# Kernel tuning notes

Measured on AMD Instinct MI355X. Metric: run time of the kernel, lower is better.

## Reference

```python
import jax, jax.numpy as jnp
import numpy as np

N_NODES = 100000
N_EDGES = 1600000
IN_CH = 48
OUT_CH = 48
BN_EPS = 1e-5


def setup_inputs() -> dict:
    key = jax.random.key(0)
    k1, k2, k3, k4 = jax.random.split(key, 4)
    x = jax.random.normal(k1, (N_NODES, IN_CH), dtype=jnp.float32)
    edge_index = jax.random.randint(k2, (2, N_EDGES), 0, N_NODES, dtype=jnp.int32)
    # GCNConv linear weight (glorot) and bias
    W = jax.random.normal(k3, (IN_CH, OUT_CH), dtype=jnp.float32) * (1.0 / np.sqrt(IN_CH))
    b = jnp.zeros((OUT_CH,), dtype=jnp.float32)
    # BatchNorm affine params
    gamma = jnp.ones((OUT_CH,), dtype=jnp.float32)
    beta = jnp.zeros((OUT_CH,), dtype=jnp.float32)
    return {"x": x, "edge_index": edge_index, "W": W, "b": b, "gamma": gamma, "beta": beta}


def reference(x, edge_index, W, b, gamma, beta):
    N = x.shape[0]
    # --- GCNConv: add self loops ---
    loops = jnp.arange(N, dtype=edge_index.dtype)
    src = jnp.concatenate([edge_index[0], loops])
    dst = jnp.concatenate([edge_index[1], loops])
    # symmetric normalization: deg counted at destination (incl. self loops)
    deg = jax.ops.segment_sum(jnp.ones_like(dst, dtype=x.dtype), dst, num_segments=N)
    dinv = jax.lax.rsqrt(deg)  # deg >= 1 due to self loops
    norm = dinv[src] * dinv[dst]  # [E+N]
    # linear transform first (small GEMM), then gather-scale-scatter
    h = x @ W  # [N, OUT_CH]
    msg = h[src] * norm[:, None]  # [E+N, OUT_CH]
    agg = jax.ops.segment_sum(msg, dst, num_segments=N) + b  # [N, OUT_CH]
    # --- BatchNorm1d (training mode: batch statistics, biased variance) ---
    mean = jnp.mean(agg, axis=0)
    var = jnp.mean(jnp.square(agg - mean), axis=0)
    y = (agg - mean) * jax.lax.rsqrt(var + BN_EPS) * gamma + beta
    # --- ReLU ---
    return jax.nn.relu(y)
```

## Files before the change

kernel.cpp:

```cpp
#include <hip/hip_runtime.h>
#include <hip/hip_bf16.h>

#define IN_CH 48
#define OUT_CH 48
#define BN_EPS 1e-5f
#define CHUNK 4096
#define EPT   16
#define NPB   256
#define NHB   512

__device__ __forceinline__ float bf2f(ushort u) {
    union { unsigned int i; float f; } v;
    v.i = ((unsigned int)u) << 16;
    return v.f;
}
__device__ __forceinline__ ushort f2bf(float f) {
    __hip_bfloat16 h = __float2bfloat16(f);
    return *(ushort*)&h;
}

__global__ __launch_bounds__(512) void k_zero(int* __restrict__ bhist) {
    bhist[threadIdx.x] = 0;
}

__global__ __launch_bounds__(256) void k_binhist(const int* __restrict__ dst,
                                                 int* __restrict__ bhist, int E) {
    __shared__ int h[512];
    int t = threadIdx.x;
    h[t] = 0; h[t + 256] = 0;
    __syncthreads();
    const int stride = NHB * 256;
    int e = blockIdx.x * 256 + t;
    for (; e + 3 * stride < E; e += 4 * stride) {
        int d0 = dst[e];
        int d1 = dst[e + stride];
        int d2 = dst[e + 2 * stride];
        int d3 = dst[e + 3 * stride];
        atomicAdd(&h[d0 >> 8], 1);
        atomicAdd(&h[d1 >> 8], 1);
        atomicAdd(&h[d2 >> 8], 1);
        atomicAdd(&h[d3 >> 8], 1);
    }
    for (; e < E; e += stride) atomicAdd(&h[dst[e] >> 8], 1);
    __syncthreads();
    if (h[t]) atomicAdd(&bhist[t], h[t]);
    if (h[t + 256]) atomicAdd(&bhist[t + 256], h[t + 256]);
}

__global__ __launch_bounds__(256) void k_scanb(const int* __restrict__ bhist,
                                               int* __restrict__ bstart,
                                               int* __restrict__ bcur, int nb,
                                               float* __restrict__ stats) {
    __shared__ int sc[256];
    int t = threadIdx.x;
    if (t < 128) stats[t] = 0.0f;
    int i0 = 2 * t, i1 = 2 * t + 1;
    int a0 = bhist[i0];
    int a1 = bhist[i1];
    int ps = a0 + a1;
    sc[t] = ps;
    __syncthreads();
    for (int off = 1; off < 256; off <<= 1) {
        int v = (t >= off) ? sc[t - off] : 0;
        __syncthreads();
        sc[t] += v;
        __syncthreads();
    }
    int excl = sc[t] - ps;
    bstart[i0] = excl;
    bstart[i1] = excl + a0;
    if (i0 < nb) bcur[i0] = excl;
    if (i1 < nb) bcur[i1] = excl + a0;
    if (t == 255) bstart[512] = sc[255];
}

union alignas(16) SMem {
    struct {
        int hist[512];
        int hbase[513];
        int sc[256];
        int gb[512];
        unsigned int stage[CHUNK];
        short stagebk[CHUNK];
    } bin;
    float Wl[IN_CH * OUT_CH];
};

__global__ __launch_bounds__(256) void k_binmm(const int* __restrict__ src,
                                               const int* __restrict__ dst,
                                               int* __restrict__ bcur,
                                               unsigned int* __restrict__ binned,
                                               int E, int nchunks,
                                               const float* __restrict__ x,
                                               const float* __restrict__ W,
                                               ushort* __restrict__ g, int N) {
    __shared__ SMem sm;
    int t = threadIdx.x;

    if (blockIdx.x < nchunks) {
        int e0 = blockIdx.x * CHUNK;
        int n = min(CHUNK, E - e0);

        sm.bin.hist[t] = 0; sm.bin.hist[t + 256] = 0;
        __syncthreads();

        unsigned int w[EPT];
        short bb[EPT];
#pragma unroll
        for (int k = 0; k < EPT; ++k) {
            int i = t + k * 256;
            if (i < n) {
                int e = e0 + i;
                int s = src[e], d = dst[e];
                int b = d >> 8;
                w[k] = (unsigned int)s | ((unsigned int)(d & 255) << 17);
                bb[k] = (short)b;
                atomicAdd(&sm.bin.hist[b], 1);
            } else bb[k] = -1;
        }
        __syncthreads();
        int a0 = sm.bin.hist[2 * t], a1 = sm.bin.hist[2 * t + 1];
        int ps = a0 + a1;
        sm.bin.sc[t] = ps;
        __syncthreads();
        for (int off = 1; off < 256; off <<= 1) {
            int v = (t >= off) ? sm.bin.sc[t - off] : 0;
            __syncthreads();
            sm.bin.sc[t] += v;
            __syncthreads();
        }
        int excl = sm.bin.sc[t] - ps;
        sm.bin.hbase[2 * t] = excl;
        sm.bin.hbase[2 * t + 1] = excl + a0;
        if (t == 255) sm.bin.hbase[512] = sm.bin.sc[255];
        __syncthreads();
        sm.bin.hist[2 * t] = excl;
        sm.bin.hist[2 * t + 1] = excl + a0;
        __syncthreads();
#pragma unroll
        for (int k = 0; k < EPT; ++k) {
            if (bb[k] >= 0) {
                int pos = atomicAdd(&sm.bin.hist[bb[k]], 1);
                sm.bin.stage[pos] = w[k];
                sm.bin.stagebk[pos] = bb[k];
            }
        }
        __syncthreads();
        for (int b = t; b < 512; b += 256) {
            int cnt = sm.bin.hbase[b + 1] - sm.bin.hbase[b];
            if (cnt > 0) sm.bin.gb[b] = atomicAdd(&bcur[b], cnt) - sm.bin.hbase[b];
        }
        __syncthreads();
        for (int j = t; j < n; j += 256) {
            int bk = sm.bin.stagebk[j];
            binned[sm.bin.gb[bk] + j] = sm.bin.stage[j];
        }
    } else {
        for (int idx = t; idx < IN_CH * OUT_CH / 4; idx += 256)
            ((float4*)sm.Wl)[idx] = ((const float4*)W)[idx];
        __syncthreads();

        int i = (blockIdx.x - nchunks) * 256 + t;
        if (i >= N) return;

        float xr[IN_CH];
        const float4* xp = (const float4*)(x + (size_t)i * IN_CH);
#pragma unroll
        for (int k = 0; k < IN_CH / 4; ++k) {
            float4 v = xp[k];
            xr[4 * k] = v.x; xr[4 * k + 1] = v.y; xr[4 * k + 2] = v.z; xr[4 * k + 3] = v.w;
        }

        ushort row[OUT_CH];
#pragma unroll
        for (int c4 = 0; c4 < OUT_CH / 4; ++c4) {
            float4 acc = make_float4(0.f, 0.f, 0.f, 0.f);
#pragma unroll
            for (int k = 0; k < IN_CH; ++k) {
                float4 wv = ((const float4*)sm.Wl)[k * (OUT_CH / 4) + c4];
                acc.x += xr[k] * wv.x; acc.y += xr[k] * wv.y;
                acc.z += xr[k] * wv.z; acc.w += xr[k] * wv.w;
            }
            row[4 * c4 + 0] = f2bf(acc.x);
            row[4 * c4 + 1] = f2bf(acc.y);
            row[4 * c4 + 2] = f2bf(acc.z);
            row[4 * c4 + 3] = f2bf(acc.w);
        }
        uint4* gp = (uint4*)(g + (size_t)i * OUT_CH);
#pragma unroll
        for (int j = 0; j < 6; ++j) gp[j] = ((uint4*)row)[j];
    }
}

__global__ __launch_bounds__(512) void k_fine(const unsigned int* __restrict__ binned,
                                              const int* __restrict__ bstart,
                                              int* __restrict__ counts,
                                              int* __restrict__ rowstart,
                                              int* __restrict__ sorted_src,
                                              ushort* __restrict__ g, int N) {
    __shared__ int cnt[256];
    __shared__ int sc[256];
    __shared__ int cur[256];
    __shared__ float sdinv[256];
    int b = blockIdx.x, t = threadIdx.x;
    int node0 = b << 8;
    int nn = min(NPB, N - node0);
    if (t < 256) cnt[t] = 0;
    __syncthreads();
    int e0 = bstart[b], e1 = bstart[b + 1];
    for (int e = e0 + t; e < e1; e += 512)
        atomicAdd(&cnt[binned[e] >> 17], 1);
    __syncthreads();
    if (t < 256) sc[t] = cnt[t];
    __syncthreads();
    for (int off = 1; off < 256; off <<= 1) {
        int v = 0;
        if (t < 256 && t >= off) v = sc[t - off];
        __syncthreads();
        if (t < 256) sc[t] += v;
        __syncthreads();
    }
    if (t < 256) {
        int excl = sc[t] - cnt[t];
        cur[t] = e0 + excl;
        sdinv[t] = rsqrtf((float)cnt[t] + 1.0f);
        if (t < nn) {
            counts[node0 + t] = cnt[t];
            rowstart[node0 + t] = e0 + excl;
        }
    }
    __syncthreads();
    for (int e = e0 + t; e < e1; e += 512) {
        unsigned int w = binned[e];
        int dl = (int)(w >> 17);
        int pos = atomicAdd(&cur[dl], 1);
        sorted_src[pos] = (int)(w & 0x1ffff);
    }
    unsigned int* gw = (unsigned int*)(g + (size_t)node0 * OUT_CH);
    int words = nn * (OUT_CH / 2);
    for (int i = t; i < words; i += 512) {
        int r = i / (OUT_CH / 2);
        float d = sdinv[r];
        unsigned int u = gw[i];
        float lo = bf2f((ushort)(u & 0xffff)) * d;
        float hi = bf2f((ushort)(u >> 16)) * d;
        gw[i] = (unsigned int)f2bf(lo) | ((unsigned int)f2bf(hi) << 16);
    }
}

__global__ __launch_bounds__(256) void k_gather(const int* __restrict__ sorted_src,
                                                const int* __restrict__ rowstart,
                                                const int* __restrict__ counts,
                                                const ushort* __restrict__ g,
                                                float* __restrict__ out, int N) {
    int t = blockIdx.x * blockDim.x + threadIdx.x;
    if (t >= N * 12) return;
    int node = t / 12;
    int sub = t - node * 12;
    const uint2* gp = (const uint2*)g;
    int cnt = counts[node];
    int e = rowstart[node];
    int end = e + cnt;

    uint2 sv = gp[(size_t)node * 12 + sub];
    float a0 = bf2f((ushort)(sv.x & 0xffff));
    float a1 = bf2f((ushort)(sv.x >> 16));
    float a2 = bf2f((ushort)(sv.y & 0xffff));
    float a3 = bf2f((ushort)(sv.y >> 16));

    for (; e + 8 <= end; e += 8) {
        int s0 = sorted_src[e];
        int s1 = sorted_src[e + 1];
        int s2 = sorted_src[e + 2];
        int s3 = sorted_src[e + 3];
        int s4 = sorted_src[e + 4];
        int s5 = sorted_src[e + 5];
        int s6 = sorted_src[e + 6];
        int s7 = sorted_src[e + 7];
        uint2 v0 = gp[(size_t)s0 * 12 + sub];
        uint2 v1 = gp[(size_t)s1 * 12 + sub];
        uint2 v2 = gp[(size_t)s2 * 12 + sub];
        uint2 v3 = gp[(size_t)s3 * 12 + sub];
        uint2 v4 = gp[(size_t)s4 * 12 + sub];
        uint2 v5 = gp[(size_t)s5 * 12 + sub];
        uint2 v6 = gp[(size_t)s6 * 12 + sub];
        uint2 v7 = gp[(size_t)s7 * 12 + sub];
        a0 += (bf2f((ushort)(v0.x & 0xffff)) + bf2f((ushort)(v1.x & 0xffff)))
            + (bf2f((ushort)(v2.x & 0xffff)) + bf2f((ushort)(v3.x & 0xffff)))
            + (bf2f((ushort)(v4.x & 0xffff)) + bf2f((ushort)(v5.x & 0xffff)))
            + (bf2f((ushort)(v6.x & 0xffff)) + bf2f((ushort)(v7.x & 0xffff)));
        a1 += (bf2f((ushort)(v0.x >> 16)) + bf2f((ushort)(v1.x >> 16)))
            + (bf2f((ushort)(v2.x >> 16)) + bf2f((ushort)(v3.x >> 16)))
            + (bf2f((ushort)(v4.x >> 16)) + bf2f((ushort)(v5.x >> 16)))
            + (bf2f((ushort)(v6.x >> 16)) + bf2f((ushort)(v7.x >> 16)));
        a2 += (bf2f((ushort)(v0.y & 0xffff)) + bf2f((ushort)(v1.y & 0xffff)))
            + (bf2f((ushort)(v2.y & 0xffff)) + bf2f((ushort)(v3.y & 0xffff)))
            + (bf2f((ushort)(v4.y & 0xffff)) + bf2f((ushort)(v5.y & 0xffff)))
            + (bf2f((ushort)(v6.y & 0xffff)) + bf2f((ushort)(v7.y & 0xffff)));
        a3 += (bf2f((ushort)(v0.y >> 16)) + bf2f((ushort)(v1.y >> 16)))
            + (bf2f((ushort)(v2.y >> 16)) + bf2f((ushort)(v3.y >> 16)))
            + (bf2f((ushort)(v4.y >> 16)) + bf2f((ushort)(v5.y >> 16)))
            + (bf2f((ushort)(v6.y >> 16)) + bf2f((ushort)(v7.y >> 16)));
    }
    for (; e + 4 <= end; e += 4) {
        int s0 = sorted_src[e];
        int s1 = sorted_src[e + 1];
        int s2 = sorted_src[e + 2];
        int s3 = sorted_src[e + 3];
        uint2 v0 = gp[(size_t)s0 * 12 + sub];
        uint2 v1 = gp[(size_t)s1 * 12 + sub];
        uint2 v2 = gp[(size_t)s2 * 12 + sub];
        uint2 v3 = gp[(size_t)s3 * 12 + sub];
        a0 += bf2f((ushort)(v0.x & 0xffff)) + bf2f((ushort)(v1.x & 0xffff))
            + bf2f((ushort)(v2.x & 0xffff)) + bf2f((ushort)(v3.x & 0xffff));
        a1 += bf2f((ushort)(v0.x >> 16)) + bf2f((ushort)(v1.x >> 16))
            + bf2f((ushort)(v2.x >> 16)) + bf2f((ushort)(v3.x >> 16));
        a2 += bf2f((ushort)(v0.y & 0xffff)) + bf2f((ushort)(v1.y & 0xffff))
            + bf2f((ushort)(v2.y & 0xffff)) + bf2f((ushort)(v3.y & 0xffff));
        a3 += bf2f((ushort)(v0.y >> 16)) + bf2f((ushort)(v1.y >> 16))
            + bf2f((ushort)(v2.y >> 16)) + bf2f((ushort)(v3.y >> 16));
    }
    for (; e < end; ++e) {
        int s = sorted_src[e];
        uint2 v = gp[(size_t)s * 12 + sub];
        a0 += bf2f((ushort)(v.x & 0xffff));
        a1 += bf2f((ushort)(v.x >> 16));
        a2 += bf2f((ushort)(v.y & 0xffff));
        a3 += bf2f((ushort)(v.y >> 16));
    }
    float di = rsqrtf((float)cnt + 1.0f);
    float4 r;
    r.x = a0 * di; r.y = a1 * di; r.z = a2 * di; r.w = a3 * di;
    ((float4*)out)[(size_t)node * 12 + sub] = r;
}

__global__ __launch_bounds__(768) void k_stats(const float* __restrict__ v,
                                               float* __restrict__ stats, int N) {
    __shared__ float ls[16][OUT_CH];
    __shared__ float ls2[16][OUT_CH];
    int c = threadIdx.x;
    int ty = threadIdx.y;
    float s = 0.f, s2 = 0.f;
    for (int r = blockIdx.x * 16 + ty; r < N; r += gridDim.x * 16) {
        float u = v[(size_t)r * OUT_CH + c];
        s += u;
        s2 += u * u;
    }
    ls[ty][c] = s;
    ls2[ty][c] = s2;
    __syncthreads();
    for (int h = 8; h > 0; h >>= 1) {
        if (ty < h) {
            ls[ty][c] += ls[ty + h][c];
            ls2[ty][c] += ls2[ty + h][c];
        }
        __syncthreads();
    }
    if (ty == 0) {
        atomicAdd(&stats[c], ls[0][c]);
        atomicAdd(&stats[OUT_CH + c], ls2[0][c]);
    }
}

__global__ void k_final(float* __restrict__ out, const float* __restrict__ stats,
                        const float* __restrict__ gamma,
                        const float* __restrict__ beta, int N) {
    int t = blockIdx.x * blockDim.x + threadIdx.x;
    int total = N * OUT_CH;
    if (t >= total) return;
    int c = t % OUT_CH;
    float invN = 1.0f / (float)N;
    float m = stats[c] * invN;
    float var = stats[OUT_CH + c] * invN - m * m;
    float y = (out[t] - m) * rsqrtf(var + BN_EPS) * gamma[c] + beta[c];
    out[t] = fmaxf(y, 0.0f);
}

extern "C" void kernel_launch(void* const* d_in, const int* in_sizes, int n_in,
                              void* d_out, int out_size, void* d_ws, size_t ws_size,
                              hipStream_t stream) {
    const float* x     = (const float*)d_in[0];
    const int*   ei    = (const int*)d_in[1];
    const float* W     = (const float*)d_in[2];
    const float* gamma = (const float*)d_in[4];
    const float* beta  = (const float*)d_in[5];
    float*       out   = (float*)d_out;

    int N = in_sizes[0] / IN_CH;
    int E = in_sizes[1] / 2;
    const int* src = ei;
    const int* dst = ei + E;

    int nb = (N + NPB - 1) / NPB;

    char* wsb = (char*)d_ws;
    float*        stats      = (float*)wsb;
    int*          bstart     = (int*)(wsb + 512);
    int*          bcur       = (int*)(wsb + 4096);
    int*          bhist      = (int*)(wsb + 8192);
    size_t A = 139264;
    int*          counts     = (int*)(wsb + A);
    int*          rowstart   = (int*)(wsb + A + (size_t)4 * N);
    unsigned int* binned     = (unsigned int*)(wsb + A + (size_t)8 * N);
    int*          sorted_src = (int*)(wsb + A + (size_t)8 * N + (size_t)4 * E);
    ushort*       g          = (ushort*)(wsb + A + (size_t)8 * N + (size_t)8 * E);

    int b = 256;
    int nchunks = (E + CHUNK - 1) / CHUNK;
    int ngemm = (N + b - 1) / b;

    k_zero<<<1, 512, 0, stream>>>(bhist);
    k_binhist<<<NHB, b, 0, stream>>>(dst, bhist, E);
    k_scanb<<<1, b, 0, stream>>>(bhist, bstart, bcur, nb, stats);
    k_binmm<<<nchunks + ngemm, b, 0, stream>>>(src, dst, bcur, binned, E, nchunks,
                                               x, W, g, N);
    k_fine<<<nb, 512, 0, stream>>>(binned, bstart, counts, rowstart, sorted_src, g, N);
    int gthreads = N * 12;
    k_gather<<<(gthreads + b - 1) / b, b, 0, stream>>>(sorted_src, rowstart, counts, g, out, N);
    dim3 sblk(OUT_CH, 16);
    k_stats<<<256, sblk, 0, stream>>>(out, stats, N);
    int totalT = N * OUT_CH;
    k_final<<<(totalT + b - 1) / b, b, 0, stream>>>(out, stats, gamma, beta, N);
}
```

Before: 129.3 us.

## Split bf16 feature table into three channel slabs and gather each in its own pass

The transformed feature table g is stored as three planar slabs of 16 channels each instead of 48-channel rows. The gather kernel runs three times, once per slab, so each pass touches a working set a third the size, which is meant to fit better in cache during random neighbour gathers. Index loads and output stores now use nontemporal hints, and the 4-wide remainder loop is removed. The cost is reading the CSR index arrays three times and two extra kernel launches.

Measured after the change: 164.1 us. 26.9% more time.

```diff
diff --git a/kernel.cpp b/kernel.cpp
--- a/kernel.cpp
+++ b/kernel.cpp
@@ -186,9 +186,12 @@
             row[4 * c4 + 2] = f2bf(acc.z);
             row[4 * c4 + 3] = f2bf(acc.w);
         }
-        uint4* gp = (uint4*)(g + (size_t)i * OUT_CH);
-#pragma unroll
-        for (int j = 0; j < 6; ++j) gp[j] = ((uint4*)row)[j];
+#pragma unroll
+        for (int p = 0; p < 3; ++p) {
+            uint4* gp = (uint4*)(g + ((size_t)p * N + i) * 16);
+            gp[0] = ((uint4*)row)[2 * p];
+            gp[1] = ((uint4*)row)[2 * p + 1];
+        }
     }
 }
 
@@ -236,55 +239,58 @@
         int pos = atomicAdd(&cur[dl], 1);
         sorted_src[pos] = (int)(w & 0x1ffff);
     }
-    unsigned int* gw = (unsigned int*)(g + (size_t)node0 * OUT_CH);
-    int words = nn * (OUT_CH / 2);
-    for (int i = t; i < words; i += 512) {
-        int r = i / (OUT_CH / 2);
-        float d = sdinv[r];
-        unsigned int u = gw[i];
-        float lo = bf2f((ushort)(u & 0xffff)) * d;
-        float hi = bf2f((ushort)(u >> 16)) * d;
-        gw[i] = (unsigned int)f2bf(lo) | ((unsigned int)f2bf(hi) << 16);
-    }
-}
-
-__global__ __launch_bounds__(256) void k_gather(const int* __restrict__ sorted_src,
-                                                const int* __restrict__ rowstart,
-                                                const int* __restrict__ counts,
-                                                const ushort* __restrict__ g,
-                                                float* __restrict__ out, int N) {
+    for (int p = 0; p < 3; ++p) {
+        unsigned int* gw = (unsigned int*)(g + ((size_t)p * N + node0) * 16);
+        int words = nn * 8;
+        for (int i = t; i < words; i += 512) {
+            int r = i >> 3;
+            float d = sdinv[r];
+            unsigned int u = gw[i];
+            float lo = bf2f((ushort)(u & 0xffff)) * d;
+            float hi = bf2f((ushort)(u >> 16)) * d;
+            gw[i] = (unsigned int)f2bf(lo) | ((unsigned int)f2bf(hi) << 16);
+        }
+    }
+}
+
+__global__ __launch_bounds__(256) void k_gather3(const int* __restrict__ sorted_src,
+                                                 const int* __restrict__ rowstart,
+                                                 const int* __restrict__ counts,
+                                                 const ushort* __restrict__ g,
+                                                 float* __restrict__ out,
+                                                 int N, int part) {
     int t = blockIdx.x * blockDim.x + threadIdx.x;
-    if (t >= N * 12) return;
-    int node = t / 12;
-    int sub = t - node * 12;
-    const uint2* gp = (const uint2*)g;
+    if (t >= N * 4) return;
+    int node = t >> 2;
+    int sub = t & 3;
+    const uint2* gp = (const uint2*)(g + ((size_t)part * N) * 16);
     int cnt = counts[node];
     int e = rowstart[node];
     int end = e + cnt;
 
-    uint2 sv = gp[(size_t)node * 12 + sub];
+    uint2 sv = gp[(size_t)node * 4 + sub];
     float a0 = bf2f((ushort)(sv.x & 0xffff));
     float a1 = bf2f((ushort)(sv.x >> 16));
     float a2 = bf2f((ushort)(sv.y & 0xffff));
     float a3 = bf2f((ushort)(sv.y >> 16));
 
     for (; e + 8 <= end; e += 8) {
-        int s0 = sorted_src[e];
-        int s1 = sorted_src[e + 1];
-        int s2 = sorted_src[e + 2];
-        int s3 = sorted_src[e + 3];
-        int s4 = sorted_src[e + 4];
-        int s5 = sorted_src[e + 5];
-        int s6 = sorted_src[e + 6];
-        int s7 = sorted_src[e + 7];
-        uint2 v0 = gp[(size_t)s0 * 12 + sub];
-        uint2 v1 = gp[(size_t)s1 * 12 + sub];
-        uint2 v2 = gp[(size_t)s2 * 12 + sub];
-        uint2 v3 = gp[(size_t)s3 * 12 + sub];
-        uint2 v4 = gp[(size_t)s4 * 12 + sub];
-        uint2 v5 = gp[(size_t)s5 * 12 + sub];
-        uint2 v6 = gp[(size_t)s6 * 12 + sub];
-        uint2 v7 = gp[(size_t)s7 * 12 + sub];
+        int s0 = __builtin_nontemporal_load(&sorted_src[e]);
+        int s1 = __builtin_nontemporal_load(&sorted_src[e + 1]);
+        int s2 = __builtin_nontemporal_load(&sorted_src[e + 2]);
+        int s3 = __builtin_nontemporal_load(&sorted_src[e + 3]);
+        int s4 = __builtin_nontemporal_load(&sorted_src[e + 4]);
+        int s5 = __builtin_nontemporal_load(&sorted_src[e + 5]);
+        int s6 = __builtin_nontemporal_load(&sorted_src[e + 6]);
+        int s7 = __builtin_nontemporal_load(&sorted_src[e + 7]);
+        uint2 v0 = gp[(size_t)s0 * 4 + sub];
+        uint2 v1 = gp[(size_t)s1 * 4 + sub];
+        uint2 v2 = gp[(size_t)s2 * 4 + sub];
+        uint2 v3 = gp[(size_t)s3 * 4 + sub];
+        uint2 v4 = gp[(size_t)s4 * 4 + sub];
+        uint2 v5 = gp[(size_t)s5 * 4 + sub];
+        uint2 v6 = gp[(size_t)s6 * 4 + sub];
+        uint2 v7 = gp[(size_t)s7 * 4 + sub];
         a0 += (bf2f((ushort)(v0.x & 0xffff)) + bf2f((ushort)(v1.x & 0xffff)))
             + (bf2f((ushort)(v2.x & 0xffff)) + bf2f((ushort)(v3.x & 0xffff)))
             + (bf2f((ushort)(v4.x & 0xffff)) + bf2f((ushort)(v5.x & 0xffff)))
@@ -302,36 +308,20 @@
             + (bf2f((ushort)(v4.y >> 16)) + bf2f((ushort)(v5.y >> 16)))
             + (bf2f((ushort)(v6.y >> 16)) + bf2f((ushort)(v7.y >> 16)));
     }
-    for (; e + 4 <= end; e += 4) {
-        int s0 = sorted_src[e];
-        int s1 = sorted_src[e + 1];
-        int s2 = sorted_src[e + 2];
-        int s3 = sorted_src[e + 3];
-        uint2 v0 = gp[(size_t)s0 * 12 + sub];
-        uint2 v1 = gp[(size_t)s1 * 12 + sub];
-        uint2 v2 = gp[(size_t)s2 * 12 + sub];
-        uint2 v3 = gp[(size_t)s3 * 12 + sub];
-        a0 += bf2f((ushort)(v0.x & 0xffff)) + bf2f((ushort)(v1.x & 0xffff))
-            + bf2f((ushort)(v2.x & 0xffff)) + bf2f((ushort)(v3.x & 0xffff));
-        a1 += bf2f((ushort)(v0.x >> 16)) + bf2f((ushort)(v1.x >> 16))
-            + bf2f((ushort)(v2.x >> 16)) + bf2f((ushort)(v3.x >> 16));
-        a2 += bf2f((ushort)(v0.y & 0xffff)) + bf2f((ushort)(v1.y & 0xffff))
-            + bf2f((ushort)(v2.y & 0xffff)) + bf2f((ushort)(v3.y & 0xffff));
-        a3 += bf2f((ushort)(v0.y >> 16)) + bf2f((ushort)(v1.y >> 16))
-            + bf2f((ushort)(v2.y >> 16)) + bf2f((ushort)(v3.y >> 16));
-    }
     for (; e < end; ++e) {
-        int s = sorted_src[e];
-        uint2 v = gp[(size_t)s * 12 + sub];
+        int s = __builtin_nontemporal_load(&sorted_src[e]);
+        uint2 v = gp[(size_t)s * 4 + sub];
         a0 += bf2f((ushort)(v.x & 0xffff));
         a1 += bf2f((ushort)(v.x >> 16));
         a2 += bf2f((ushort)(v.y & 0xffff));
         a3 += bf2f((ushort)(v.y >> 16));
     }
     float di = rsqrtf((float)cnt + 1.0f);
-    float4 r;
-    r.x = a0 * di; r.y = a1 * di; r.z = a2 * di; r.w = a3 * di;
-    ((float4*)out)[(size_t)node * 12 + sub] = r;
+    union { float f[4]; unsigned long long u[2]; } cv;
+    cv.f[0] = a0 * di; cv.f[1] = a1 * di; cv.f[2] = a2 * di; cv.f[3] = a3 * di;
+    float* op = out + (size_t)node * OUT_CH + part * 16 + sub * 4;
+    __builtin_nontemporal_store(cv.u[0], (unsigned long long*)op);
+    __builtin_nontemporal_store(cv.u[1], (unsigned long long*)(op + 2));
 }
 
 __global__ __launch_bounds__(768) void k_stats(const float* __restrict__ v,
@@ -415,8 +405,10 @@
     k_binmm<<<nchunks + ngemm, b, 0, stream>>>(src, dst, bcur, binned, E, nchunks,
                                                x, W, g, N);
     k_fine<<<nb, 512, 0, stream>>>(binned, bstart, counts, rowstart, sorted_src, g, N);
-    int gthreads = N * 12;
-    k_gather<<<(gthreads + b - 1) / b, b, 0, stream>>>(sorted_src, rowstart, counts, g, out, N);
+    int gthreads = N * 4;
+    int gblocks = (gthreads + b - 1) / b;
+    for (int p = 0; p < 3; ++p)
+        k_gather3<<<gblocks, b, 0, stream>>>(sorted_src, rowstart, counts, g, out, N, p);
     dim3 sblk(OUT_CH, 16);
     k_stats<<<256, sblk, 0, stream>>>(out, stats, N);
     int totalT = N * OUT_CH;
```

## Fuse BatchNorm statistics into gather kernel with per-block partials and reduction

Applied to the files above, without the earlier changes.

The gather kernel now accumulates per-channel sum and sum-of-squares in shared memory with LDS atomics and writes one partial per block. A small reduction kernel then combines the partials into the stats buffer, which replaces the separate stats pass and the global atomic zeroing. This avoids re-reading the full fp32 output (about 19MB) to compute batch statistics. In exchange it adds shared-memory atomic contention inside the gather, a partials buffer, and an extra small launch.

Result: slower. 162.5 us (+25.7%).

```diff
diff --git a/kernel.cpp b/kernel.cpp
--- a/kernel.cpp
+++ b/kernel.cpp
@@ -49,11 +49,9 @@
 
 __global__ __launch_bounds__(256) void k_scanb(const int* __restrict__ bhist,
                                                int* __restrict__ bstart,
-                                               int* __restrict__ bcur, int nb,
-                                               float* __restrict__ stats) {
+                                               int* __restrict__ bcur, int nb) {
     __shared__ int sc[256];
     int t = threadIdx.x;
-    if (t < 128) stats[t] = 0.0f;
     int i0 = 2 * t, i1 = 2 * t + 1;
     int a0 = bhist[i0];
     int a1 = bhist[i1];
@@ -252,114 +250,124 @@
                                                 const int* __restrict__ rowstart,
                                                 const int* __restrict__ counts,
                                                 const ushort* __restrict__ g,
-                                                float* __restrict__ out, int N) {
-    int t = blockIdx.x * blockDim.x + threadIdx.x;
-    if (t >= N * 12) return;
-    int node = t / 12;
-    int sub = t - node * 12;
-    const uint2* gp = (const uint2*)g;
-    int cnt = counts[node];
-    int e = rowstart[node];
-    int end = e + cnt;
-
-    uint2 sv = gp[(size_t)node * 12 + sub];
-    float a0 = bf2f((ushort)(sv.x & 0xffff));
-    float a1 = bf2f((ushort)(sv.x >> 16));
-    float a2 = bf2f((ushort)(sv.y & 0xffff));
-    float a3 = bf2f((ushort)(sv.y >> 16));
-
-    for (; e + 8 <= end; e += 8) {
-        int s0 = sorted_src[e];
-        int s1 = sorted_src[e + 1];
-        int s2 = sorted_src[e + 2];
-        int s3 = sorted_src[e + 3];
-        int s4 = sorted_src[e + 4];
-        int s5 = sorted_src[e + 5];
-        int s6 = sorted_src[e + 6];
-        int s7 = sorted_src[e + 7];
-        uint2 v0 = gp[(size_t)s0 * 12 + sub];
-        uint2 v1 = gp[(size_t)s1 * 12 + sub];
-        uint2 v2 = gp[(size_t)s2 * 12 + sub];
-        uint2 v3 = gp[(size_t)s3 * 12 + sub];
-        uint2 v4 = gp[(size_t)s4 * 12 + sub];
-        uint2 v5 = gp[(size_t)s5 * 12 + sub];
-        uint2 v6 = gp[(size_t)s6 * 12 + sub];
-        uint2 v7 = gp[(size_t)s7 * 12 + sub];
-        a0 += (bf2f((ushort)(v0.x & 0xffff)) + bf2f((ushort)(v1.x & 0xffff)))
-            + (bf2f((ushort)(v2.x & 0xffff)) + bf2f((ushort)(v3.x & 0xffff)))
-            + (bf2f((ushort)(v4.x & 0xffff)) + bf2f((ushort)(v5.x & 0xffff)))
-            + (bf2f((ushort)(v6.x & 0xffff)) + bf2f((ushort)(v7.x & 0xffff)));
-        a1 += (bf2f((ushort)(v0.x >> 16)) + bf2f((ushort)(v1.x >> 16)))
-            + (bf2f((ushort)(v2.x >> 16)) + bf2f((ushort)(v3.x >> 16)))
-            + (bf2f((ushort)(v4.x >> 16)) + bf2f((ushort)(v5.x >> 16)))
-            + (bf2f((ushort)(v6.x >> 16)) + bf2f((ushort)(v7.x >> 16)));
-        a2 += (bf2f((ushort)(v0.y & 0xffff)) + bf2f((ushort)(v1.y & 0xffff)))
-            + (bf2f((ushort)(v2.y & 0xffff)) + bf2f((ushort)(v3.y & 0xffff)))
-            + (bf2f((ushort)(v4.y & 0xffff)) + bf2f((ushort)(v5.y & 0xffff)))
-            + (bf2f((ushort)(v6.y & 0xffff)) + bf2f((ushort)(v7.y & 0xffff)));
-        a3 += (bf2f((ushort)(v0.y >> 16)) + bf2f((ushort)(v1.y >> 16)))
-            + (bf2f((ushort)(v2.y >> 16)) + bf2f((ushort)(v3.y >> 16)))
-            + (bf2f((ushort)(v4.y >> 16)) + bf2f((ushort)(v5.y >> 16)))
-            + (bf2f((ushort)(v6.y >> 16)) + bf2f((ushort)(v7.y >> 16)));
-    }
-    for (; e + 4 <= end; e += 4) {
-        int s0 = sorted_src[e];
-        int s1 = sorted_src[e + 1];
-        int s2 = sorted_src[e + 2];
-        int s3 = sorted_src[e + 3];
-        uint2 v0 = gp[(size_t)s0 * 12 + sub];
-        uint2 v1 = gp[(size_t)s1 * 12 + sub];
-        uint2 v2 = gp[(size_t)s2 * 12 + sub];
-        uint2 v3 = gp[(size_t)s3 * 12 + sub];
-        a0 += bf2f((ushort)(v0.x & 0xffff)) + bf2f((ushort)(v1.x & 0xffff))
-            + bf2f((ushort)(v2.x & 0xffff)) + bf2f((ushort)(v3.x & 0xffff));
-        a1 += bf2f((ushort)(v0.x >> 16)) + bf2f((ushort)(v1.x >> 16))
-            + bf2f((ushort)(v2.x >> 16)) + bf2f((ushort)(v3.x >> 16));
-        a2 += bf2f((ushort)(v0.y & 0xffff)) + bf2f((ushort)(v1.y & 0xffff))
-            + bf2f((ushort)(v2.y & 0xffff)) + bf2f((ushort)(v3.y & 0xffff));
-        a3 += bf2f((ushort)(v0.y >> 16)) + bf2f((ushort)(v1.y >> 16))
-            + bf2f((ushort)(v2.y >> 16)) + bf2f((ushort)(v3.y >> 16));
-    }
-    for (; e < end; ++e) {
-        int s = sorted_src[e];
-        uint2 v = gp[(size_t)s * 12 + sub];
-        a0 += bf2f((ushort)(v.x & 0xffff));
-        a1 += bf2f((ushort)(v.x >> 16));
-        a2 += bf2f((ushort)(v.y & 0xffff));
-        a3 += bf2f((ushort)(v.y >> 16));
-    }
-    float di = rsqrtf((float)cnt + 1.0f);
-    float4 r;
-    r.x = a0 * di; r.y = a1 * di; r.z = a2 * di; r.w = a3 * di;
-    ((float4*)out)[(size_t)node * 12 + sub] = r;
-}
-
-__global__ __launch_bounds__(768) void k_stats(const float* __restrict__ v,
-                                               float* __restrict__ stats, int N) {
-    __shared__ float ls[16][OUT_CH];
-    __shared__ float ls2[16][OUT_CH];
-    int c = threadIdx.x;
-    int ty = threadIdx.y;
-    float s = 0.f, s2 = 0.f;
-    for (int r = blockIdx.x * 16 + ty; r < N; r += gridDim.x * 16) {
-        float u = v[(size_t)r * OUT_CH + c];
-        s += u;
-        s2 += u * u;
-    }
-    ls[ty][c] = s;
-    ls2[ty][c] = s2;
-    __syncthreads();
-    for (int h = 8; h > 0; h >>= 1) {
-        if (ty < h) {
-            ls[ty][c] += ls[ty + h][c];
-            ls2[ty][c] += ls2[ty + h][c];
-        }
-        __syncthreads();
-    }
-    if (ty == 0) {
-        atomicAdd(&stats[c], ls[0][c]);
-        atomicAdd(&stats[OUT_CH + c], ls2[0][c]);
-    }
+                                                float* __restrict__ out,
+                                                float* __restrict__ spart, int N) {
+    __shared__ float ssum[OUT_CH];
+    __shared__ float ssq[OUT_CH];
+    int lt = threadIdx.x;
+    if (lt < OUT_CH) { ssum[lt] = 0.0f; ssq[lt] = 0.0f; }
+    __syncthreads();
+
+    int t = blockIdx.x * 256 + lt;
+    if (t < N * 12) {
+        int node = t / 12;
+        int sub = t - node * 12;
+        const uint2* gp = (const uint2*)g;
+        int cnt = counts[node];
+        int e = rowstart[node];
+        int end = e + cnt;
+
+        uint2 sv = gp[(size_t)node * 12 + sub];
+        float a0 = bf2f((ushort)(sv.x & 0xffff));
+        float a1 = bf2f((ushort)(sv.x >> 16));
+        float a2 = bf2f((ushort)(sv.y & 0xffff));
+        float a3 = bf2f((ushort)(sv.y >> 16));
+
+        for (; e + 8 <= end; e += 8) {
+            int s0 = sorted_src[e];
+            int s1 = sorted_src[e + 1];
+            int s2 = sorted_src[e + 2];
+            int s3 = sorted_src[e + 3];
+            int s4 = sorted_src[e + 4];
+            int s5 = sorted_src[e + 5];
+            int s6 = sorted_src[e + 6];
+            int s7 = sorted_src[e + 7];
+            uint2 v0 = gp[(size_t)s0 * 12 + sub];
+            uint2 v1 = gp[(size_t)s1 * 12 + sub];
+            uint2 v2 = gp[(size_t)s2 * 12 + sub];
+            uint2 v3 = gp[(size_t)s3 * 12 + sub];
+            uint2 v4 = gp[(size_t)s4 * 12 + sub];
+            uint2 v5 = gp[(size_t)s5 * 12 + sub];
+            uint2 v6 = gp[(size_t)s6 * 12 + sub];
+            uint2 v7 = gp[(size_t)s7 * 12 + sub];
+            a0 += (bf2f((ushort)(v0.x & 0xffff)) + bf2f((ushort)(v1.x & 0xffff)))
+                + (bf2f((ushort)(v2.x & 0xffff)) + bf2f((ushort)(v3.x & 0xffff)))
+                + (bf2f((ushort)(v4.x & 0xffff)) + bf2f((ushort)(v5.x & 0xffff)))
+                + (bf2f((ushort)(v6.x & 0xffff)) + bf2f((ushort)(v7.x & 0xffff)));
+            a1 += (bf2f((ushort)(v0.x >> 16)) + bf2f((ushort)(v1.x >> 16)))
+                + (bf2f((ushort)(v2.x >> 16)) + bf2f((ushort)(v3.x >> 16)))
+                + (bf2f((ushort)(v4.x >> 16)) + bf2f((ushort)(v5.x >> 16)))
+                + (bf2f((ushort)(v6.x >> 16)) + bf2f((ushort)(v7.x >> 16)));
+            a2 += (bf2f((ushort)(v0.y & 0xffff)) + bf2f((ushort)(v1.y & 0xffff)))
+                + (bf2f((ushort)(v2.y & 0xffff)) + bf2f((ushort)(v3.y & 0xffff)))
+                + (bf2f((ushort)(v4.y & 0xffff)) + bf2f((ushort)(v5.y & 0xffff)))
+                + (bf2f((ushort)(v6.y & 0xffff)) + bf2f((ushort)(v7.y & 0xffff)));
+            a3 += (bf2f((ushort)(v0.y >> 16)) + bf2f((ushort)(v1.y >> 16)))
+                + (bf2f((ushort)(v2.y >> 16)) + bf2f((ushort)(v3.y >> 16)))
+                + (bf2f((ushort)(v4.y >> 16)) + bf2f((ushort)(v5.y >> 16)))
+                + (bf2f((ushort)(v6.y >> 16)) + bf2f((ushort)(v7.y >> 16)));
+        }
+        for (; e + 4 <= end; e += 4) {
+            int s0 = sorted_src[e];
+            int s1 = sorted_src[e + 1];
+            int s2 = sorted_src[e + 2];
+            int s3 = sorted_src[e + 3];
+            uint2 v0 = gp[(size_t)s0 * 12 + sub];
+            uint2 v1 = gp[(size_t)s1 * 12 + sub];
+            uint2 v2 = gp[(size_t)s2 * 12 + sub];
+            uint2 v3 = gp[(size_t)s3 * 12 + sub];
+            a0 += bf2f((ushort)(v0.x & 0xffff)) + bf2f((ushort)(v1.x & 0xffff))
+                + bf2f((ushort)(v2.x & 0xffff)) + bf2f((ushort)(v3.x & 0xffff));
+            a1 += bf2f((ushort)(v0.x >> 16)) + bf2f((ushort)(v1.x >> 16))
+                + bf2f((ushort)(v2.x >> 16)) + bf2f((ushort)(v3.x >> 16));
+            a2 += bf2f((ushort)(v0.y & 0xffff)) + bf2f((ushort)(v1.y & 0xffff))
+                + bf2f((ushort)(v2.y & 0xffff)) + bf2f((ushort)(v3.y & 0xffff));
+            a3 += bf2f((ushort)(v0.y >> 16)) + bf2f((ushort)(v1.y >> 16))
+                + bf2f((ushort)(v2.y >> 16)) + bf2f((ushort)(v3.y >> 16));
+        }
+        for (; e < end; ++e) {
+            int s = sorted_src[e];
+            uint2 v = gp[(size_t)s * 12 + sub];
+            a0 += bf2f((ushort)(v.x & 0xffff));
+            a1 += bf2f((ushort)(v.x >> 16));
+            a2 += bf2f((ushort)(v.y & 0xffff));
+            a3 += bf2f((ushort)(v.y >> 16));
+        }
+        float di = rsqrtf((float)cnt + 1.0f);
+        float4 r;
+        r.x = a0 * di; r.y = a1 * di; r.z = a2 * di; r.w = a3 * di;
+        ((float4*)out)[(size_t)node * 12 + sub] = r;
+        int c = 4 * sub;
+        atomicAdd(&ssum[c + 0], r.x);
+        atomicAdd(&ssum[c + 1], r.y);
+        atomicAdd(&ssum[c + 2], r.z);
+        atomicAdd(&ssum[c + 3], r.w);
+        atomicAdd(&ssq[c + 0], r.x * r.x);
+        atomicAdd(&ssq[c + 1], r.y * r.y);
+        atomicAdd(&ssq[c + 2], r.z * r.z);
+        atomicAdd(&ssq[c + 3], r.w * r.w);
+    }
+    __syncthreads();
+    if (lt < OUT_CH) {
+        spart[(size_t)blockIdx.x * 96 + lt] = ssum[lt];
+        spart[(size_t)blockIdx.x * 96 + OUT_CH + lt] = ssq[lt];
+    }
+}
+
+__global__ __launch_bounds__(256) void k_redstats(const float* __restrict__ spart,
+                                                  float* __restrict__ stats, int nblk) {
+    __shared__ float l[256];
+    int c = blockIdx.x;
+    int t = threadIdx.x;
+    float s = 0.f;
+    for (int b = t; b < nblk; b += 256) s += spart[(size_t)b * 96 + c];
+    l[t] = s;
+    __syncthreads();
+    for (int h = 128; h > 0; h >>= 1) {
+        if (t < h) l[t] += l[t + h];
+        __syncthreads();
+    }
+    if (t == 0) stats[c] = l[0];
 }
 
 __global__ void k_final(float* __restrict__ out, const float* __restrict__ stats,
@@ -404,6 +412,7 @@
     unsigned int* binned     = (unsigned int*)(wsb + A + (size_t)8 * N);
     int*          sorted_src = (int*)(wsb + A + (size_t)8 * N + (size_t)4 * E);
     ushort*       g          = (ushort*)(wsb + A + (size_t)8 * N + (size_t)8 * E);
+    float*        spart      = (float*)(wsb + A + (size_t)8 * N + (size_t)8 * E + (size_t)96 * N);
 
     int b = 256;
     int nchunks = (E + CHUNK - 1) / CHUNK;
@@ -411,14 +420,14 @@
 
     k_zero<<<1, 512, 0, stream>>>(bhist);
     k_binhist<<<NHB, b, 0, stream>>>(dst, bhist, E);
-    k_scanb<<<1, b, 0, stream>>>(bhist, bstart, bcur, nb, stats);
+    k_scanb<<<1, b, 0, stream>>>(bhist, bstart, bcur, nb);
     k_binmm<<<nchunks + ngemm, b, 0, stream>>>(src, dst, bcur, binned, E, nchunks,
                                                x, W, g, N);
     k_fine<<<nb, 512, 0, stream>>>(binned, bstart, counts, rowstart, sorted_src, g, N);
     int gthreads = N * 12;
-    k_gather<<<(gthreads + b - 1) / b, b, 0, stream>>>(sorted_src, rowstart, counts, g, out, N);
-    dim3 sblk(OUT_CH, 16);
-    k_stats<<<256, sblk, 0, stream>>>(out, stats, N);
+    int gblocks = (gthreads + b - 1) / b;
+    k_gather<<<gblocks, b, 0, stream>>>(sorted_src, rowstart, counts, g, out, spart, N);
+    k_redstats<<<2 * OUT_CH, b, 0, stream>>>(spart, stats, gblocks);
     int totalT = N * OUT_CH;
     k_final<<<(totalT + b - 1) / b, b, 0, stream>>>(out, stats, gamma, beta, N);
 }
```
